# Performance work log

Hardware: AMD Instinct MI355X
Metric: run time of the kernel (lower is better)

Reference implementation:

```python
import jax, jax.numpy as jnp
import numpy as np

LN_EPS = 1e-5

def setup_inputs() -> dict:
    key = jax.random.key(0)
    k1, k2, k3 = jax.random.split(key, 3)
    B, Lq, Lk, D = 16, 2048, 2048, 128
    return {
        "query": jax.random.normal(k1, (B, Lq, D), dtype=jnp.float32),
        "key": jax.random.normal(k2, (B, Lk, D), dtype=jnp.float32),
        "value": jax.random.normal(k3, (B, Lk, D), dtype=jnp.float32),
        "attn_mask": jnp.zeros((Lq, Lk), dtype=jnp.float32),
        "gamma": jnp.ones((D,), dtype=jnp.float32),
        "beta": jnp.zeros((D,), dtype=jnp.float32),
    }

def reference(query, key, value, attn_mask, gamma, beta):
    # NOTE: original code does NOT scale by 1/sqrt(d) despite the class name.
    scores = jnp.einsum("bqd,bkd->bqk", query, key)          # [B,Lq,Lk]
    scores = scores + attn_mask[None, :, :]
    probs = jax.nn.softmax(scores, axis=-1)
    out = jnp.einsum("bqk,bkd->bqd", probs, value)            # [B,Lq,D]
    # dropout is identity (eval / rate 0)
    mu = jnp.mean(out, axis=-1, keepdims=True)
    var = jnp.var(out, axis=-1, keepdims=True)
    normed = (out - mu) * jax.lax.rsqrt(var + LN_EPS)
    return normed * gamma + beta
```

## Files before the change

### kernel.cpp

```cpp
#include <hip/hip_runtime.h>
#include <hip/hip_bf16.h>
#include <hip/hip_fp16.h>
#include <math.h>

#define LQ_  2048
#define LK_  2048
#define D_   128
#define B_   16
#define LN_EPS 1e-5f
#define TK_  32
#define NTILE (LK_ / TK_)

#define KH_TILE_US 4096
#define VT_TILE_U  2048
#define KH_BYTES   ((size_t)B_ * NTILE * KH_TILE_US * 2)
#define VT_OFF     KH_BYTES

typedef __attribute__((ext_vector_type(8))) short short8;
typedef __attribute__((ext_vector_type(8))) _Float16 half8;
typedef __attribute__((ext_vector_type(4))) float f32x4;

union FragU { uint4 u4; short8 s8; half8 h8; unsigned int u[4]; };

__device__ __forceinline__ unsigned int pk_bf16(float a, float b) {
  __hip_bfloat162 h = __float22bfloat162_rn(make_float2(a, b));
  unsigned int u;
  __builtin_memcpy(&u, &h, 4);
  return u;
}
__device__ __forceinline__ unsigned int pk_f16(float a, float b) {
  __half2 h = __floats2half2_rn(a, b);
  unsigned int u;
  __builtin_memcpy(&u, &h, 4);
  return u;
}
__device__ __forceinline__ float f16_lo(unsigned int u) {
  unsigned short s = (unsigned short)(u & 0xffffu);
  __half h; __builtin_memcpy(&h, &s, 2); return __half2float(h);
}
__device__ __forceinline__ float f16_hi(unsigned int u) {
  unsigned short s = (unsigned short)(u >> 16);
  __half h; __builtin_memcpy(&h, &s, 2); return __half2float(h);
}

__device__ __forceinline__ int idxK(int row, int d) {
  return row * 128 + ((((d >> 3) ^ row) & 15) << 3) + (d & 7);
}
__device__ __forceinline__ int idxVt(int d, int slot) {
  return d * 16 + ((((slot >> 2) + (d >> 1)) & 3) << 2) + (slot & 3);
}

__device__ __forceinline__ void barrier_stage() {
  asm volatile("s_waitcnt vmcnt(2) lgkmcnt(0)\n\ts_barrier" ::: "memory");
}

__device__ __forceinline__ void gld_lds16(const void* g, void* l) {
  __builtin_amdgcn_global_load_lds((const __attribute__((address_space(1))) void*)g,
                                   (__attribute__((address_space(3))) void*)l, 16, 0, 0);
}

__global__ __launch_bounds__(256) void conv_kv(
    const float* __restrict__ kg, const float* __restrict__ vg,
    unsigned short* __restrict__ khg, unsigned int* __restrict__ vtg)
{
  __shared__ float Vlt[128 * 33];
  const int tid = threadIdx.x;
  const int blk = blockIdx.x;
  const int b = blk >> 6;
  const int t = blk & 63;

  const float* ks = kg + ((size_t)b * LK_ + t * 32) * D_;
  const float* vs = vg + ((size_t)b * LK_ + t * 32) * D_;
  unsigned short* kh = khg + (size_t)blk * KH_TILE_US;
  unsigned int*   vt = vtg + (size_t)blk * VT_TILE_U;

#pragma unroll
  for (int it = 0; it < 2; it++) {
    const int item = tid + it * 256;
    const int row = item >> 4;
    const int c8  = item & 15;
    const float* p = ks + row * D_ + c8 * 8;
    float4 x = *(const float4*)(p);
    float4 y = *(const float4*)(p + 4);
    FragU H;
    H.u[0] = pk_f16(x.x, x.y); H.u[1] = pk_f16(x.z, x.w);
    H.u[2] = pk_f16(y.x, y.y); H.u[3] = pk_f16(y.z, y.w);
    *(uint4*)&kh[idxK(row, c8 * 8)] = H.u4;
  }

#pragma unroll
  for (int i = 0; i < 4; i++) {
    const int item = tid + i * 256;
    const int r = item >> 5, c4 = item & 31;
    float4 x = *(const float4*)&vs[r * D_ + c4 * 4];
    Vlt[(c4 * 4 + 0) * 33 + r] = x.x;
    Vlt[(c4 * 4 + 1) * 33 + r] = x.y;
    Vlt[(c4 * 4 + 2) * 33 + r] = x.z;
    Vlt[(c4 * 4 + 3) * 33 + r] = x.w;
  }
  __syncthreads();

#pragma unroll
  for (int i = 0; i < 8; i++) {
    const int o = tid + i * 256;
    const int d = o >> 4, sp = o & 15;
    const int gl = ((sp >> 2) - (d >> 1)) & 3;
    const int c  = sp & 3;
    const int kp = 2 * gl + ((c >> 1) << 3) + (c & 1);
    vt[o] = pk_bf16(Vlt[d * 33 + 2 * kp], Vlt[d * 33 + 2 * kp + 1]);
  }
}

__device__ __forceinline__ void stage_tile(int w, int lane,
    const unsigned short* khT, const unsigned int* vtT,
    int tile, char* khs, char* vts)
{
  const char* gkh = (const char*)(khT + (size_t)tile * KH_TILE_US);
  const char* gvt = (const char*)(vtT + (size_t)tile * VT_TILE_U);
#pragma unroll
  for (int c = 0; c < 2; c++) {
    const int off = (w + 4 * c) << 10;
    gld_lds16(gkh + off + lane * 16, khs + off);
    gld_lds16(gvt + off + lane * 16, vts + off);
  }
}

__global__ __launch_bounds__(256, 2) void attn_ln_mfma(
    const float* __restrict__ qg, const float* __restrict__ maskg,
    const float* __restrict__ gammag, const float* __restrict__ betag,
    const unsigned short* __restrict__ khg, const unsigned int* __restrict__ vtg,
    float* __restrict__ outg)
{
  __shared__ unsigned short KhS[2][32 * 128];
  __shared__ unsigned int   VtW[2][128 * 16];

  const int tid  = threadIdx.x;
  const int w    = tid >> 6;
  const int lane = tid & 63;
  const int quad = lane >> 4;
  const int lr   = lane & 15;

  const int id   = blockIdx.x;
  const int xcd  = id & 7;
  const int slot = id >> 3;
  const int b    = xcd * 2 + (slot >> 5);
  const int q0   = (slot & 31) * 64;

  const unsigned short* khT = khg + (size_t)b * NTILE * KH_TILE_US;
  const unsigned int*   vtT = vtg + (size_t)b * NTILE * VT_TILE_U;

  const float* mrow = maskg + (size_t)(q0 + w * 16 + lr) * LK_ + quad * 4;

  stage_tile(w, lane, khT, vtT, 0, (char*)&KhS[0][0], (char*)&VtW[0][0]);
  float4 mA[2], mB[2];
  mA[0] = *(const float4*)(mrow);
  mA[1] = *(const float4*)(mrow + 16);

  half8 qh[4], ql[4];
  {
    const float* qrow = qg + ((size_t)b * LQ_ + q0 + w * 16 + lr) * D_ + quad * 8;
#pragma unroll
    for (int c = 0; c < 4; c++) {
      float4 x = *(const float4*)(qrow + c * 32);
      float4 y = *(const float4*)(qrow + c * 32 + 4);
      FragU H, L;
      H.u[0] = pk_f16(x.x, x.y); H.u[1] = pk_f16(x.z, x.w);
      H.u[2] = pk_f16(y.x, y.y); H.u[3] = pk_f16(y.z, y.w);
      L.u[0] = pk_f16(x.x - f16_lo(H.u[0]), x.y - f16_hi(H.u[0]));
      L.u[1] = pk_f16(x.z - f16_lo(H.u[1]), x.w - f16_hi(H.u[1]));
      L.u[2] = pk_f16(y.x - f16_lo(H.u[2]), y.y - f16_hi(H.u[2]));
      L.u[3] = pk_f16(y.z - f16_lo(H.u[3]), y.w - f16_hi(H.u[3]));
      qh[c] = H.h8; ql[c] = L.h8;
    }
  }

  float l_part = 0.f;
  f32x4 o[8];
  const f32x4 zf = {0.f, 0.f, 0.f, 0.f};
#pragma unroll
  for (int n = 0; n < 8; n++) o[n] = zf;

  auto body = [&](int kt, int cur, float4 (&mu)[2], float4 (&mp)[2])
      __attribute__((always_inline)) -> void {
    const unsigned short* khc = &KhS[cur][0];
    const unsigned int*   vtc = &VtW[cur][0];

    barrier_stage();

    if (kt + 1 < NTILE) {
      stage_tile(w, lane, khT, vtT, kt + 1,
                 (char*)&KhS[cur ^ 1][0], (char*)&VtW[cur ^ 1][0]);
      mp[0] = *(const float4*)(mrow + (kt + 1) * TK_);
      mp[1] = *(const float4*)(mrow + (kt + 1) * TK_ + 16);
    }

    f32x4 sH[2], sL[2];
    sH[0] = zf; sH[1] = zf; sL[0] = zf; sL[1] = zf;
#pragma unroll
    for (int c = 0; c < 4; c++) {
#pragma unroll
      for (int ct = 0; ct < 2; ct++) {
        FragU kh;
        kh.u4 = *(const uint4*)&khc[idxK(ct * 16 + lr, c * 32 + quad * 8)];
        sH[ct] = __builtin_amdgcn_mfma_f32_16x16x32_f16(kh.h8, qh[c], sH[ct], 0, 0, 0);
        sL[ct] = __builtin_amdgcn_mfma_f32_16x16x32_f16(kh.h8, ql[c], sL[ct], 0, 0, 0);
      }
    }

    FragU Bv[8];
#pragma unroll
    for (int nb = 0; nb < 8; nb++)
      Bv[nb].u4 = *(const uint4*)&vtc[idxVt(nb * 16 + lr, quad * 4)];

    float pv[2][4];
#pragma unroll
    for (int ct = 0; ct < 2; ct++) {
      const float* mf = (const float*)&mu[ct];
#pragma unroll
      for (int reg = 0; reg < 4; reg++) {
        float p = __expf(sH[ct][reg] + sL[ct][reg] + mf[reg]);
        l_part += p;
        pv[ct][reg] = p;
      }
    }

    FragU A;
    A.u[0] = pk_bf16(pv[0][0], pv[0][1]);
    A.u[1] = pk_bf16(pv[0][2], pv[0][3]);
    A.u[2] = pk_bf16(pv[1][0], pv[1][1]);
    A.u[3] = pk_bf16(pv[1][2], pv[1][3]);

#pragma unroll
    for (int nb = 0; nb < 8; nb++)
      o[nb] = __builtin_amdgcn_mfma_f32_16x16x32_bf16(A.s8, Bv[nb].s8, o[nb], 0, 0, 0);
  };

  for (int kt = 0; kt < NTILE; kt += 2) {
    body(kt,     0, mA, mB);
    body(kt + 1, 1, mB, mA);
  }

  float lt = l_part;
  lt += __shfl_xor(lt, 16, 64);
  lt += __shfl_xor(lt, 32, 64);
  const float invl = 1.f / lt;

  float inv_l[4];
#pragma unroll
  for (int reg = 0; reg < 4; reg++)
    inv_l[reg] = __shfl(invl, quad * 20 + reg, 64);

  float gam[8], bet[8];
#pragma unroll
  for (int nb = 0; nb < 8; nb++) {
    gam[nb] = gammag[nb * 16 + lr];
    bet[nb] = betag[nb * 16 + lr];
  }

#pragma unroll
  for (int reg = 0; reg < 4; reg++) {
    float s1 = 0.f, s2 = 0.f;
#pragma unroll
    for (int nb = 0; nb < 8; nb++) {
      float v = o[nb][reg] * inv_l[reg];
      o[nb][reg] = v;
      s1 += v; s2 += v * v;
    }
#pragma unroll
    for (int m = 1; m <= 8; m <<= 1) {
      s1 += __shfl_xor(s1, m, 64);
      s2 += __shfl_xor(s2, m, 64);
    }
    const float mean = s1 * (1.f / 128.f);
    const float var  = s2 * (1.f / 128.f) - mean * mean;
    const float rstd = rsqrtf(var + LN_EPS);

    float* op = outg + ((size_t)b * LQ_ + q0 + w * 16 + quad * 4 + reg) * D_ + lr;
#pragma unroll
    for (int nb = 0; nb < 8; nb++)
      op[nb * 16] = (o[nb][reg] - mean) * rstd * gam[nb] + bet[nb];
  }
}

extern "C" void kernel_launch(void* const* d_in, const int* in_sizes, int n_in,
                              void* d_out, int out_size, void* d_ws, size_t ws_size,
                              hipStream_t stream) {
  const float* q     = (const float*)d_in[0];
  const float* k     = (const float*)d_in[1];
  const float* v     = (const float*)d_in[2];
  const float* mask  = (const float*)d_in[3];
  const float* gamma = (const float*)d_in[4];
  const float* beta  = (const float*)d_in[5];
  float* out = (float*)d_out;

  unsigned short* khg = (unsigned short*)d_ws;
  unsigned int*   vtg = (unsigned int*)((char*)d_ws + VT_OFF);

  conv_kv<<<dim3(B_ * NTILE), dim3(256), 0, stream>>>(k, v, khg, vtg);
  attn_ln_mfma<<<dim3(512), dim3(256), 0, stream>>>(q, mask, gamma, beta,
                                                    khg, vtg, out);
}
```

Baseline: 182.0 us.

## Load K/V fragments directly from global into registers, dropping LDS staging

The preprocessing kernel now writes K in a fragment-ordered layout, so each lane of the attention kernel can load its MFMA operands straight from global memory into registers. The LDS double buffer, global_load_lds staging and per-tile barriers are removed. Register double-buffering of K fragments and sched_barrier placement are meant to overlap the loads with MFMA work. The cost is higher register pressure and that every wave independently re-reads the same K/V tile from global/L2 instead of sharing it through LDS.

```diff
diff --git a/kernel.cpp b/kernel.cpp
--- a/kernel.cpp
+++ b/kernel.cpp
@@ -11,9 +11,9 @@
 #define TK_  32
 #define NTILE (LK_ / TK_)
 
-#define KH_TILE_US 4096
-#define VT_TILE_U  2048
-#define KH_BYTES   ((size_t)B_ * NTILE * KH_TILE_US * 2)
+#define KH_TILE_B  8192
+#define VT_TILE_B  8192
+#define KH_BYTES   ((size_t)B_ * NTILE * KH_TILE_B)
 #define VT_OFF     KH_BYTES
 
 typedef __attribute__((ext_vector_type(8))) short short8;
@@ -43,20 +43,8 @@
   __half h; __builtin_memcpy(&h, &s, 2); return __half2float(h);
 }
 
-__device__ __forceinline__ int idxK(int row, int d) {
-  return row * 128 + ((((d >> 3) ^ row) & 15) << 3) + (d & 7);
-}
 __device__ __forceinline__ int idxVt(int d, int slot) {
   return d * 16 + ((((slot >> 2) + (d >> 1)) & 3) << 2) + (slot & 3);
-}
-
-__device__ __forceinline__ void barrier_stage() {
-  asm volatile("s_waitcnt vmcnt(2) lgkmcnt(0)\n\ts_barrier" ::: "memory");
-}
-
-__device__ __forceinline__ void gld_lds16(const void* g, void* l) {
-  __builtin_amdgcn_global_load_lds((const __attribute__((address_space(1))) void*)g,
-                                   (__attribute__((address_space(3))) void*)l, 16, 0, 0);
 }
 
 __global__ __launch_bounds__(256) void conv_kv(
@@ -71,8 +59,8 @@
 
   const float* ks = kg + ((size_t)b * LK_ + t * 32) * D_;
   const float* vs = vg + ((size_t)b * LK_ + t * 32) * D_;
-  unsigned short* kh = khg + (size_t)blk * KH_TILE_US;
-  unsigned int*   vt = vtg + (size_t)blk * VT_TILE_U;
+  unsigned short* kh = khg + (size_t)blk * (KH_TILE_B / 2);
+  unsigned int*   vt = vtg + (size_t)blk * (VT_TILE_B / 4);
 
 #pragma unroll
   for (int it = 0; it < 2; it++) {
@@ -85,7 +73,9 @@
     FragU H;
     H.u[0] = pk_f16(x.x, x.y); H.u[1] = pk_f16(x.z, x.w);
     H.u[2] = pk_f16(y.x, y.y); H.u[3] = pk_f16(y.z, y.w);
-    *(uint4*)&kh[idxK(row, c8 * 8)] = H.u4;
+    const int c = c8 >> 2, quad = c8 & 3;
+    const int ct = row >> 4, lr = row & 15;
+    *(uint4*)&kh[((c * 2 + ct) << 9) + (quad * 16 + lr) * 8] = H.u4;
   }
 
 #pragma unroll
@@ -111,29 +101,12 @@
   }
 }
 
-__device__ __forceinline__ void stage_tile(int w, int lane,
-    const unsigned short* khT, const unsigned int* vtT,
-    int tile, char* khs, char* vts)
-{
-  const char* gkh = (const char*)(khT + (size_t)tile * KH_TILE_US);
-  const char* gvt = (const char*)(vtT + (size_t)tile * VT_TILE_U);
-#pragma unroll
-  for (int c = 0; c < 2; c++) {
-    const int off = (w + 4 * c) << 10;
-    gld_lds16(gkh + off + lane * 16, khs + off);
-    gld_lds16(gvt + off + lane * 16, vts + off);
-  }
-}
-
 __global__ __launch_bounds__(256, 2) void attn_ln_mfma(
     const float* __restrict__ qg, const float* __restrict__ maskg,
     const float* __restrict__ gammag, const float* __restrict__ betag,
     const unsigned short* __restrict__ khg, const unsigned int* __restrict__ vtg,
     float* __restrict__ outg)
 {
-  __shared__ unsigned short KhS[2][32 * 128];
-  __shared__ unsigned int   VtW[2][128 * 16];
-
   const int tid  = threadIdx.x;
   const int w    = tid >> 6;
   const int lane = tid & 63;
@@ -146,15 +119,35 @@
   const int b    = xcd * 2 + (slot >> 5);
   const int q0   = (slot & 31) * 64;
 
-  const unsigned short* khT = khg + (size_t)b * NTILE * KH_TILE_US;
-  const unsigned int*   vtT = vtg + (size_t)b * NTILE * VT_TILE_U;
+  const char* khT = (const char*)khg + (size_t)b * NTILE * KH_TILE_B;
+  const char* vtT = (const char*)vtg + (size_t)b * NTILE * VT_TILE_B;
+
+  const int kOff = lane * 16;
+  const int vOff = idxVt(lr, quad * 4) * 4;
 
   const float* mrow = maskg + (size_t)(q0 + w * 16 + lr) * LK_ + quad * 4;
 
-  stage_tile(w, lane, khT, vtT, 0, (char*)&KhS[0][0], (char*)&VtW[0][0]);
+  FragU kfA[8], kfB[8], vf[8];
   float4 mA[2], mB[2];
-  mA[0] = *(const float4*)(mrow);
-  mA[1] = *(const float4*)(mrow + 16);
+
+  auto loadK = [&](int kt, FragU (&kf)[8]) __attribute__((always_inline)) {
+    const char* p = khT + (size_t)kt * KH_TILE_B + kOff;
+#pragma unroll
+    for (int f = 0; f < 8; f++) kf[f].u4 = *(const uint4*)(p + (f << 10));
+  };
+  auto loadV = [&](int kt) __attribute__((always_inline)) {
+    const char* p = vtT + (size_t)kt * VT_TILE_B + vOff;
+#pragma unroll
+    for (int nb = 0; nb < 8; nb++) vf[nb].u4 = *(const uint4*)(p + (nb << 10));
+  };
+  auto loadM = [&](int kt, float4 (&m)[2]) __attribute__((always_inline)) {
+    m[0] = *(const float4*)(mrow + kt * TK_);
+    m[1] = *(const float4*)(mrow + kt * TK_ + 16);
+  };
+
+  loadK(0, kfA);
+  loadM(0, mA);
+  loadV(0);
 
   half8 qh[4], ql[4];
   {
@@ -180,37 +173,25 @@
 #pragma unroll
   for (int n = 0; n < 8; n++) o[n] = zf;
 
-  auto body = [&](int kt, int cur, float4 (&mu)[2], float4 (&mp)[2])
+  auto body = [&](int kt, FragU (&kfC)[8], FragU (&kfN)[8],
+                  float4 (&mu)[2], float4 (&mp)[2])
       __attribute__((always_inline)) -> void {
-    const unsigned short* khc = &KhS[cur][0];
-    const unsigned int*   vtc = &VtW[cur][0];
-
-    barrier_stage();
-
-    if (kt + 1 < NTILE) {
-      stage_tile(w, lane, khT, vtT, kt + 1,
-                 (char*)&KhS[cur ^ 1][0], (char*)&VtW[cur ^ 1][0]);
-      mp[0] = *(const float4*)(mrow + (kt + 1) * TK_);
-      mp[1] = *(const float4*)(mrow + (kt + 1) * TK_ + 16);
-    }
+    if (kt + 1 < NTILE) loadK(kt + 1, kfN);
+    __builtin_amdgcn_sched_barrier(0);
 
     f32x4 sH[2], sL[2];
     sH[0] = zf; sH[1] = zf; sL[0] = zf; sL[1] = zf;
 #pragma unroll
-    for (int c = 0; c < 4; c++) {
+    for (int c = 0; c < 4; c++)
 #pragma unroll
       for (int ct = 0; ct < 2; ct++) {
-        FragU kh;
-        kh.u4 = *(const uint4*)&khc[idxK(ct * 16 + lr, c * 32 + quad * 8)];
-        sH[ct] = __builtin_amdgcn_mfma_f32_16x16x32_f16(kh.h8, qh[c], sH[ct], 0, 0, 0);
-        sL[ct] = __builtin_amdgcn_mfma_f32_16x16x32_f16(kh.h8, ql[c], sL[ct], 0, 0, 0);
+        const int f = c * 2 + ct;
+        sH[ct] = __builtin_amdgcn_mfma_f32_16x16x32_f16(kfC[f].h8, qh[c], sH[ct], 0, 0, 0);
+        sL[ct] = __builtin_amdgcn_mfma_f32_16x16x32_f16(kfC[f].h8, ql[c], sL[ct], 0, 0, 0);
       }
-    }
-
-    FragU Bv[8];
-#pragma unroll
-    for (int nb = 0; nb < 8; nb++)
-      Bv[nb].u4 = *(const uint4*)&vtc[idxVt(nb * 16 + lr, quad * 4)];
+
+    if (kt + 1 < NTILE) loadM(kt + 1, mp);
+    __builtin_amdgcn_sched_barrier(0);
 
     float pv[2][4];
 #pragma unroll
@@ -232,12 +213,15 @@
 
 #pragma unroll
     for (int nb = 0; nb < 8; nb++)
-      o[nb] = __builtin_amdgcn_mfma_f32_16x16x32_bf16(A.s8, Bv[nb].s8, o[nb], 0, 0, 0);
+      o[nb] = __builtin_amdgcn_mfma_f32_16x16x32_bf16(A.s8, vf[nb].s8, o[nb], 0, 0, 0);
+
+    if (kt + 1 < NTILE) loadV(kt + 1);
+    __builtin_amdgcn_sched_barrier(0);
   };
 
   for (int kt = 0; kt < NTILE; kt += 2) {
-    body(kt,     0, mA, mB);
-    body(kt + 1, 1, mB, mA);
+    body(kt,     kfA, kfB, mA, mB);
+    body(kt + 1, kfB, kfA, mB, mA);
   }
 
   float lt = l_part;
```

Result: slower. 202.5 us (+11.3%).

## Stage key/value tiles in pairs per barrier and use exp2 with prescaled queries

Applied to the files above, without the earlier changes.

Each pipeline stage now loads two 32-key tiles at once into doubled LDS buffers, which halves the number of barriers and staging rounds per block. Queries are prescaled by log2(e) so the softmax exponent can use exp2f, with the mask term folded in through an fmaf. The cost is twice the LDS footprint, which may reduce occupancy, and more in-flight loads, reflected in the larger vmcnt wait threshold.

```diff
diff --git a/kernel.cpp b/kernel.cpp
--- a/kernel.cpp
+++ b/kernel.cpp
@@ -10,6 +10,8 @@
 #define LN_EPS 1e-5f
 #define TK_  32
 #define NTILE (LK_ / TK_)
+#define NPAIR (NTILE / 2)
+#define LOG2E 1.4426950408889634f
 
 #define KH_TILE_US 4096
 #define VT_TILE_U  2048
@@ -51,7 +53,7 @@
 }
 
 __device__ __forceinline__ void barrier_stage() {
-  asm volatile("s_waitcnt vmcnt(2) lgkmcnt(0)\n\ts_barrier" ::: "memory");
+  asm volatile("s_waitcnt vmcnt(4) lgkmcnt(0)\n\ts_barrier" ::: "memory");
 }
 
 __device__ __forceinline__ void gld_lds16(const void* g, void* l) {
@@ -111,14 +113,14 @@
   }
 }
 
-__device__ __forceinline__ void stage_tile(int w, int lane,
+__device__ __forceinline__ void stage_pair(int w, int lane,
     const unsigned short* khT, const unsigned int* vtT,
-    int tile, char* khs, char* vts)
+    int tp, char* khs, char* vts)
 {
-  const char* gkh = (const char*)(khT + (size_t)tile * KH_TILE_US);
-  const char* gvt = (const char*)(vtT + (size_t)tile * VT_TILE_U);
-#pragma unroll
-  for (int c = 0; c < 2; c++) {
+  const char* gkh = (const char*)khT + (size_t)tp * 16384;
+  const char* gvt = (const char*)vtT + (size_t)tp * 16384;
+#pragma unroll
+  for (int c = 0; c < 4; c++) {
     const int off = (w + 4 * c) << 10;
     gld_lds16(gkh + off + lane * 16, khs + off);
     gld_lds16(gvt + off + lane * 16, vts + off);
@@ -131,8 +133,8 @@
     const unsigned short* __restrict__ khg, const unsigned int* __restrict__ vtg,
     float* __restrict__ outg)
 {
-  __shared__ unsigned short KhS[2][32 * 128];
-  __shared__ unsigned int   VtW[2][128 * 16];
+  __shared__ unsigned short KhS[2][64 * 128];
+  __shared__ unsigned int   VtW[2][64 * 64];
 
   const int tid  = threadIdx.x;
   const int w    = tid >> 6;
@@ -151,10 +153,12 @@
 
   const float* mrow = maskg + (size_t)(q0 + w * 16 + lr) * LK_ + quad * 4;
 
-  stage_tile(w, lane, khT, vtT, 0, (char*)&KhS[0][0], (char*)&VtW[0][0]);
-  float4 mA[2], mB[2];
+  stage_pair(w, lane, khT, vtT, 0, (char*)&KhS[0][0], (char*)&VtW[0][0]);
+  float4 mA[4], mB[4];
   mA[0] = *(const float4*)(mrow);
   mA[1] = *(const float4*)(mrow + 16);
+  mA[2] = *(const float4*)(mrow + 32);
+  mA[3] = *(const float4*)(mrow + 48);
 
   half8 qh[4], ql[4];
   {
@@ -163,6 +167,8 @@
     for (int c = 0; c < 4; c++) {
       float4 x = *(const float4*)(qrow + c * 32);
       float4 y = *(const float4*)(qrow + c * 32 + 4);
+      x.x *= LOG2E; x.y *= LOG2E; x.z *= LOG2E; x.w *= LOG2E;
+      y.x *= LOG2E; y.y *= LOG2E; y.z *= LOG2E; y.w *= LOG2E;
       FragU H, L;
       H.u[0] = pk_f16(x.x, x.y); H.u[1] = pk_f16(x.z, x.w);
       H.u[2] = pk_f16(y.x, y.y); H.u[3] = pk_f16(y.z, y.w);
@@ -180,24 +186,13 @@
 #pragma unroll
   for (int n = 0; n < 8; n++) o[n] = zf;
 
-  auto body = [&](int kt, int cur, float4 (&mu)[2], float4 (&mp)[2])
+  auto subtile = [&](const unsigned short* khc, const unsigned int* vtc,
+                     const float4& mu0, const float4& mu1)
       __attribute__((always_inline)) -> void {
-    const unsigned short* khc = &KhS[cur][0];
-    const unsigned int*   vtc = &VtW[cur][0];
-
-    barrier_stage();
-
-    if (kt + 1 < NTILE) {
-      stage_tile(w, lane, khT, vtT, kt + 1,
-                 (char*)&KhS[cur ^ 1][0], (char*)&VtW[cur ^ 1][0]);
-      mp[0] = *(const float4*)(mrow + (kt + 1) * TK_);
-      mp[1] = *(const float4*)(mrow + (kt + 1) * TK_ + 16);
-    }
-
     f32x4 sH[2], sL[2];
     sH[0] = zf; sH[1] = zf; sL[0] = zf; sL[1] = zf;
 #pragma unroll
-    for (int c = 0; c < 4; c++) {
+    for (int c = 0; c < 4; c++)
 #pragma unroll
       for (int ct = 0; ct < 2; ct++) {
         FragU kh;
@@ -205,7 +200,6 @@
         sH[ct] = __builtin_amdgcn_mfma_f32_16x16x32_f16(kh.h8, qh[c], sH[ct], 0, 0, 0);
         sL[ct] = __builtin_amdgcn_mfma_f32_16x16x32_f16(kh.h8, ql[c], sL[ct], 0, 0, 0);
       }
-    }
 
     FragU Bv[8];
 #pragma unroll
@@ -213,15 +207,14 @@
       Bv[nb].u4 = *(const uint4*)&vtc[idxVt(nb * 16 + lr, quad * 4)];
 
     float pv[2][4];
-#pragma unroll
-    for (int ct = 0; ct < 2; ct++) {
-      const float* mf = (const float*)&mu[ct];
-#pragma unroll
-      for (int reg = 0; reg < 4; reg++) {
-        float p = __expf(sH[ct][reg] + sL[ct][reg] + mf[reg]);
-        l_part += p;
-        pv[ct][reg] = p;
-      }
+    const float* mf0 = (const float*)&mu0;
+    const float* mf1 = (const float*)&mu1;
+#pragma unroll
+    for (int reg = 0; reg < 4; reg++) {
+      float p0 = exp2f(fmaf(mf0[reg], LOG2E, sH[0][reg] + sL[0][reg]));
+      float p1 = exp2f(fmaf(mf1[reg], LOG2E, sH[1][reg] + sL[1][reg]));
+      l_part += p0; l_part += p1;
+      pv[0][reg] = p0; pv[1][reg] = p1;
     }
 
     FragU A;
@@ -235,9 +228,30 @@
       o[nb] = __builtin_amdgcn_mfma_f32_16x16x32_bf16(A.s8, Bv[nb].s8, o[nb], 0, 0, 0);
   };
 
-  for (int kt = 0; kt < NTILE; kt += 2) {
-    body(kt,     0, mA, mB);
-    body(kt + 1, 1, mB, mA);
+  auto body = [&](int tp, int cur, float4 (&mu)[4], float4 (&mp)[4])
+      __attribute__((always_inline)) -> void {
+    const unsigned short* khc = &KhS[cur][0];
+    const unsigned int*   vtc = &VtW[cur][0];
+
+    barrier_stage();
+
+    if (tp + 1 < NPAIR) {
+      stage_pair(w, lane, khT, vtT, tp + 1,
+                 (char*)&KhS[cur ^ 1][0], (char*)&VtW[cur ^ 1][0]);
+      const float* mn = mrow + (size_t)(tp + 1) * 64;
+      mp[0] = *(const float4*)(mn);
+      mp[1] = *(const float4*)(mn + 16);
+      mp[2] = *(const float4*)(mn + 32);
+      mp[3] = *(const float4*)(mn + 48);
+    }
+
+    subtile(khc,        vtc,        mu[0], mu[1]);
+    subtile(khc + 4096, vtc + 2048, mu[2], mu[3]);
+  };
+
+  for (int tp = 0; tp < NPAIR; tp += 2) {
+    body(tp,     0, mA, mB);
+    body(tp + 1, 1, mB, mA);
   }
 
   float lt = l_part;
```

New measurement: 181.5 us. Within noise of the previous version (-0.3%).

## Process two 16-row query groups per wave to reuse staged K/V tiles

Applied to the files above, without the earlier changes.

Each wave now handles 32 query rows (two 16-row groups) instead of 16, so each block covers 128 queries and the grid halves to 256 blocks. Every K and V fragment read from LDS feeds twice as many MFMAs, which halves the global-to-LDS staging traffic per query. The waitcnt is raised to allow four outstanding mask loads, and launch bounds drop to one block per SM. In exchange register pressure roughly doubles for accumulators and Q fragments, occupancy falls, and 256 blocks may underfill the 256 CUs with less latency hiding.

```diff
diff --git a/kernel.cpp b/kernel.cpp
--- a/kernel.cpp
+++ b/kernel.cpp
@@ -51,7 +51,7 @@
 }
 
 __device__ __forceinline__ void barrier_stage() {
-  asm volatile("s_waitcnt vmcnt(2) lgkmcnt(0)\n\ts_barrier" ::: "memory");
+  asm volatile("s_waitcnt vmcnt(4) lgkmcnt(0)\n\ts_barrier" ::: "memory");
 }
 
 __device__ __forceinline__ void gld_lds16(const void* g, void* l) {
@@ -125,7 +125,7 @@
   }
 }
 
-__global__ __launch_bounds__(256, 2) void attn_ln_mfma(
+__global__ __launch_bounds__(256, 1) void attn_ln_mfma(
     const float* __restrict__ qg, const float* __restrict__ maskg,
     const float* __restrict__ gammag, const float* __restrict__ betag,
     const unsigned short* __restrict__ khg, const unsigned int* __restrict__ vtg,
@@ -143,22 +143,26 @@
   const int id   = blockIdx.x;
   const int xcd  = id & 7;
   const int slot = id >> 3;
-  const int b    = xcd * 2 + (slot >> 5);
-  const int q0   = (slot & 31) * 64;
+  const int b    = xcd * 2 + (slot >> 4);
+  const int q0   = (slot & 15) * 128;
 
   const unsigned short* khT = khg + (size_t)b * NTILE * KH_TILE_US;
   const unsigned int*   vtT = vtg + (size_t)b * NTILE * VT_TILE_U;
 
-  const float* mrow = maskg + (size_t)(q0 + w * 16 + lr) * LK_ + quad * 4;
+  const float* mrow0 = maskg + (size_t)(q0 + w * 32 + lr) * LK_ + quad * 4;
+  const float* mrow1 = mrow0 + (size_t)16 * LK_;
 
   stage_tile(w, lane, khT, vtT, 0, (char*)&KhS[0][0], (char*)&VtW[0][0]);
-  float4 mA[2], mB[2];
-  mA[0] = *(const float4*)(mrow);
-  mA[1] = *(const float4*)(mrow + 16);
-
-  half8 qh[4], ql[4];
-  {
-    const float* qrow = qg + ((size_t)b * LQ_ + q0 + w * 16 + lr) * D_ + quad * 8;
+  float4 mA[2][2], mB[2][2];
+  mA[0][0] = *(const float4*)(mrow0);
+  mA[0][1] = *(const float4*)(mrow0 + 16);
+  mA[1][0] = *(const float4*)(mrow1);
+  mA[1][1] = *(const float4*)(mrow1 + 16);
+
+  half8 qh[2][4], ql[2][4];
+#pragma unroll
+  for (int g = 0; g < 2; g++) {
+    const float* qrow = qg + ((size_t)b * LQ_ + q0 + w * 32 + g * 16 + lr) * D_ + quad * 8;
 #pragma unroll
     for (int c = 0; c < 4; c++) {
       float4 x = *(const float4*)(qrow + c * 32);
@@ -170,17 +174,19 @@
       L.u[1] = pk_f16(x.z - f16_lo(H.u[1]), x.w - f16_hi(H.u[1]));
       L.u[2] = pk_f16(y.x - f16_lo(H.u[2]), y.y - f16_hi(H.u[2]));
       L.u[3] = pk_f16(y.z - f16_lo(H.u[3]), y.w - f16_hi(H.u[3]));
-      qh[c] = H.h8; ql[c] = L.h8;
-    }
-  }
-
-  float l_part = 0.f;
-  f32x4 o[8];
+      qh[g][c] = H.h8; ql[g][c] = L.h8;
+    }
+  }
+
+  float l_part[2] = {0.f, 0.f};
+  f32x4 o[2][8];
   const f32x4 zf = {0.f, 0.f, 0.f, 0.f};
 #pragma unroll
-  for (int n = 0; n < 8; n++) o[n] = zf;
-
-  auto body = [&](int kt, int cur, float4 (&mu)[2], float4 (&mp)[2])
+  for (int g = 0; g < 2; g++)
+#pragma unroll
+    for (int n = 0; n < 8; n++) o[g][n] = zf;
+
+  auto body = [&](int kt, int cur, float4 (&mu)[2][2], float4 (&mp)[2][2])
       __attribute__((always_inline)) -> void {
     const unsigned short* khc = &KhS[cur][0];
     const unsigned int*   vtc = &VtW[cur][0];
@@ -190,49 +196,57 @@
     if (kt + 1 < NTILE) {
       stage_tile(w, lane, khT, vtT, kt + 1,
                  (char*)&KhS[cur ^ 1][0], (char*)&VtW[cur ^ 1][0]);
-      mp[0] = *(const float4*)(mrow + (kt + 1) * TK_);
-      mp[1] = *(const float4*)(mrow + (kt + 1) * TK_ + 16);
-    }
-
-    f32x4 sH[2], sL[2];
-    sH[0] = zf; sH[1] = zf; sL[0] = zf; sL[1] = zf;
-#pragma unroll
-    for (int c = 0; c < 4; c++) {
+      mp[0][0] = *(const float4*)(mrow0 + (kt + 1) * TK_);
+      mp[0][1] = *(const float4*)(mrow0 + (kt + 1) * TK_ + 16);
+      mp[1][0] = *(const float4*)(mrow1 + (kt + 1) * TK_);
+      mp[1][1] = *(const float4*)(mrow1 + (kt + 1) * TK_ + 16);
+    }
+
+    f32x4 sH[2][2], sL[2][2];
+#pragma unroll
+    for (int g = 0; g < 2; g++) {
+      sH[g][0] = zf; sH[g][1] = zf; sL[g][0] = zf; sL[g][1] = zf;
+    }
+#pragma unroll
+    for (int c = 0; c < 4; c++)
 #pragma unroll
       for (int ct = 0; ct < 2; ct++) {
         FragU kh;
         kh.u4 = *(const uint4*)&khc[idxK(ct * 16 + lr, c * 32 + quad * 8)];
-        sH[ct] = __builtin_amdgcn_mfma_f32_16x16x32_f16(kh.h8, qh[c], sH[ct], 0, 0, 0);
-        sL[ct] = __builtin_amdgcn_mfma_f32_16x16x32_f16(kh.h8, ql[c], sL[ct], 0, 0, 0);
+#pragma unroll
+        for (int g = 0; g < 2; g++) {
+          sH[g][ct] = __builtin_amdgcn_mfma_f32_16x16x32_f16(kh.h8, qh[g][c], sH[g][ct], 0, 0, 0);
+          sL[g][ct] = __builtin_amdgcn_mfma_f32_16x16x32_f16(kh.h8, ql[g][c], sL[g][ct], 0, 0, 0);
+        }
       }
-    }
 
     FragU Bv[8];
 #pragma unroll
     for (int nb = 0; nb < 8; nb++)
       Bv[nb].u4 = *(const uint4*)&vtc[idxVt(nb * 16 + lr, quad * 4)];
 
-    float pv[2][4];
-#pragma unroll
-    for (int ct = 0; ct < 2; ct++) {
-      const float* mf = (const float*)&mu[ct];
-#pragma unroll
-      for (int reg = 0; reg < 4; reg++) {
-        float p = __expf(sH[ct][reg] + sL[ct][reg] + mf[reg]);
-        l_part += p;
-        pv[ct][reg] = p;
+#pragma unroll
+    for (int g = 0; g < 2; g++) {
+      float pv[2][4];
+#pragma unroll
+      for (int ct = 0; ct < 2; ct++) {
+        const float* mf = (const float*)&mu[g][ct];
+#pragma unroll
+        for (int reg = 0; reg < 4; reg++) {
+          float p = __expf(sH[g][ct][reg] + sL[g][ct][reg] + mf[reg]);
+          l_part[g] += p;
+          pv[ct][reg] = p;
+        }
       }
-    }
-
-    FragU A;
-    A.u[0] = pk_bf16(pv[0][0], pv[0][1]);
-    A.u[1] = pk_bf16(pv[0][2], pv[0][3]);
-    A.u[2] = pk_bf16(pv[1][0], pv[1][1]);
-    A.u[3] = pk_bf16(pv[1][2], pv[1][3]);
-
-#pragma unroll
-    for (int nb = 0; nb < 8; nb++)
-      o[nb] = __builtin_amdgcn_mfma_f32_16x16x32_bf16(A.s8, Bv[nb].s8, o[nb], 0, 0, 0);
+      FragU A;
+      A.u[0] = pk_bf16(pv[0][0], pv[0][1]);
+      A.u[1] = pk_bf16(pv[0][2], pv[0][3]);
+      A.u[2] = pk_bf16(pv[1][0], pv[1][1]);
+      A.u[3] = pk_bf16(pv[1][2], pv[1][3]);
+#pragma unroll
+      for (int nb = 0; nb < 8; nb++)
+        o[g][nb] = __builtin_amdgcn_mfma_f32_16x16x32_bf16(A.s8, Bv[nb].s8, o[g][nb], 0, 0, 0);
+    }
   };
 
   for (int kt = 0; kt < NTILE; kt += 2) {
@@ -240,16 +254,6 @@
     body(kt + 1, 1, mB, mA);
   }
 
-  float lt = l_part;
-  lt += __shfl_xor(lt, 16, 64);
-  lt += __shfl_xor(lt, 32, 64);
-  const float invl = 1.f / lt;
-
-  float inv_l[4];
-#pragma unroll
-  for (int reg = 0; reg < 4; reg++)
-    inv_l[reg] = __shfl(invl, quad * 20 + reg, 64);
-
   float gam[8], bet[8];
 #pragma unroll
   for (int nb = 0; nb < 8; nb++) {
@@ -258,27 +262,40 @@
   }
 
 #pragma unroll
-  for (int reg = 0; reg < 4; reg++) {
-    float s1 = 0.f, s2 = 0.f;
-#pragma unroll
-    for (int nb = 0; nb < 8; nb++) {
-      float v = o[nb][reg] * inv_l[reg];
-      o[nb][reg] = v;
-      s1 += v; s2 += v * v;
-    }
-#pragma unroll
-    for (int m = 1; m <= 8; m <<= 1) {
-      s1 += __shfl_xor(s1, m, 64);
-      s2 += __shfl_xor(s2, m, 64);
-    }
-    const float mean = s1 * (1.f / 128.f);
-    const float var  = s2 * (1.f / 128.f) - mean * mean;
-    const float rstd = rsqrtf(var + LN_EPS);
-
-    float* op = outg + ((size_t)b * LQ_ + q0 + w * 16 + quad * 4 + reg) * D_ + lr;
-#pragma unroll
-    for (int nb = 0; nb < 8; nb++)
-      op[nb * 16] = (o[nb][reg] - mean) * rstd * gam[nb] + bet[nb];
+  for (int g = 0; g < 2; g++) {
+    float lt = l_part[g];
+    lt += __shfl_xor(lt, 16, 64);
+    lt += __shfl_xor(lt, 32, 64);
+    const float invl = 1.f / lt;
+
+    float inv_l[4];
+#pragma unroll
+    for (int reg = 0; reg < 4; reg++)
+      inv_l[reg] = __shfl(invl, quad * 20 + reg, 64);
+
+#pragma unroll
+    for (int reg = 0; reg < 4; reg++) {
+      float s1 = 0.f, s2 = 0.f;
+#pragma unroll
+      for (int nb = 0; nb < 8; nb++) {
+        float v = o[g][nb][reg] * inv_l[reg];
+        o[g][nb][reg] = v;
+        s1 += v; s2 += v * v;
+      }
+#pragma unroll
+      for (int m = 1; m <= 8; m <<= 1) {
+        s1 += __shfl_xor(s1, m, 64);
+        s2 += __shfl_xor(s2, m, 64);
+      }
+      const float mean = s1 * (1.f / 128.f);
+      const float var  = s2 * (1.f / 128.f) - mean * mean;
+      const float rstd = rsqrtf(var + LN_EPS);
+
+      float* op = outg + ((size_t)b * LQ_ + q0 + w * 32 + g * 16 + quad * 4 + reg) * D_ + lr;
+#pragma unroll
+      for (int nb = 0; nb < 8; nb++)
+        op[nb * 16] = (o[g][nb][reg] - mean) * rstd * gam[nb] + bet[nb];
+    }
   }
 }
 
@@ -297,6 +314,6 @@
   unsigned int*   vtg = (unsigned int*)((char*)d_ws + VT_OFF);
 
   conv_kv<<<dim3(B_ * NTILE), dim3(256), 0, stream>>>(k, v, khg, vtg);
-  attn_ln_mfma<<<dim3(512), dim3(256), 0, stream>>>(q, mask, gamma, beta,
+  attn_ln_mfma<<<dim3(256), dim3(256), 0, stream>>>(q, mask, gamma, beta,
                                                     khg, vtg, out);
 }
```

Result: slower. 213.2 us (+17.2%).
